# Performance work log

Hardware: AMD Instinct MI355X
Metric: run time of the kernel (lower is better)

Reference implementation:

```python
import jax, jax.numpy as jnp
import numpy as np

D_MODEL, H, DK = 768, 12, 64
RQ, RK, RV = 6, 2, 2
B, S = 8, 4096


def setup_inputs() -> dict:
    key = jax.random.key(0)
    ks = jax.random.split(key, 16)
    def lin(k, din, dout):
        k1, k2 = jax.random.split(k)
        s = 1.0 / np.sqrt(din)
        W = jax.random.uniform(k1, (din, dout), jnp.float32, -s, s)
        b = jax.random.uniform(k2, (dout,), jnp.float32, -s, s)
        return W, b
    W_a_q, b_a_q = lin(ks[0], D_MODEL, H * RQ)
    W_b_q, b_b_q = lin(ks[1], D_MODEL, DK * RQ)
    W_a_k, b_a_k = lin(ks[2], D_MODEL, H * RK)
    W_b_k, b_b_k = lin(ks[3], D_MODEL, DK * RK)
    W_a_v, b_a_v = lin(ks[4], D_MODEL, H * RV)
    W_b_v, b_b_v = lin(ks[5], D_MODEL, DK * RV)
    W_out, b_out = lin(ks[6], H * DK, D_MODEL)
    x = jax.random.normal(ks[7], (B, S, D_MODEL), jnp.float32)
    rope_pos = jax.random.normal(ks[8], (S, DK), jnp.float32)
    return {
        "x": x, "rope_pos": rope_pos,
        "W_a_q": W_a_q, "b_a_q": b_a_q, "W_b_q": W_b_q, "b_b_q": b_b_q,
        "W_a_k": W_a_k, "b_a_k": b_a_k, "W_b_k": W_b_k, "b_b_k": b_b_k,
        "W_a_v": W_a_v, "b_a_v": b_a_v, "W_b_v": W_b_v, "b_b_v": b_b_v,
        "W_out": W_out, "b_out": b_out,
    }


def reference(x, rope_pos, W_a_q, b_a_q, W_b_q, b_b_q, W_a_k, b_a_k,
              W_b_k, b_b_k, W_a_v, b_a_v, W_b_v, b_b_v, W_out, b_out):
    b, s, _ = x.shape
    # factor projections; layout (B, S, rank, feature)
    A_Q = (x @ W_a_q + b_a_q).reshape(b, s, RQ, H)
    B_Q = (x @ W_b_q + b_b_q).reshape(b, s, RQ, DK)
    A_K = (x @ W_a_k + b_a_k).reshape(b, s, RK, H)
    B_K = (x @ W_b_k + b_b_k).reshape(b, s, RK, DK)
    A_V = (x @ W_a_v + b_a_v).reshape(b, s, RV, H)
    B_V = (x @ W_b_v + b_b_v).reshape(b, s, RV, DK)
    rope = rope_pos[None, :, None, :]  # (1,S,1,DK)
    B_Q = B_Q * rope
    B_K = B_K * rope
    # rank-sum outer products -> (B,S,H,DK)
    Q = jnp.einsum('bsrh,bsrd->bshd', A_Q, B_Q)
    K = jnp.einsum('bsrh,bsrd->bshd', A_K, B_K)
    V = jnp.einsum('bsrh,bsrd->bshd', A_V, B_V)
    # faithful to original: scores over head dim, shape (B,S,H,H)
    scores = jnp.einsum('bshd,bsgd->bshg', Q, K) / jnp.sqrt(jnp.float32(DK))
    attn = jax.nn.softmax(scores, axis=-1)
    out = jnp.einsum('bshg,bsgd->bshd', attn, V)  # (B,S,H,DK)
    # faithful reshape: (B,S,H,DK) -> transpose(1,2) -> (B,H,S,DK) -> view (B,S,H*DK)
    out = jnp.transpose(out, (0, 2, 1, 3)).reshape(b, s, H * DK)
    return out @ W_out + b_out
```

## Files before the change

kernel.cpp:

```cpp
#include <hip/hip_runtime.h>
#include <hip/hip_bf16.h>

#define D_MODEL 768
#define NH 12
#define DK 64
#define RQ 6
#define RK 2
#define RV 2
#define BATCH 8
#define SEQ 4096
#define NPOS (BATCH*SEQ)

typedef _Float16 v8h __attribute__((ext_vector_type(8)));
typedef float v4f __attribute__((ext_vector_type(4)));

#define GLDS16(ldst, gsrc)                                                     \
    __builtin_amdgcn_global_load_lds(                                          \
        (const __attribute__((address_space(1))) void*)(unsigned long long)    \
            (const void*)(gsrc),                                               \
        (__attribute__((address_space(3))) void*)(unsigned int)                \
            (unsigned long long)(void*)(ldst),                                 \
        16, 0, 0)

__global__ __launch_bounds__(256) void repack(
    const float* __restrict__ Waq, const float* __restrict__ baq,
    const float* __restrict__ Wbq, const float* __restrict__ bbq,
    const float* __restrict__ Wak, const float* __restrict__ bak,
    const float* __restrict__ Wbk, const float* __restrict__ bbk,
    const float* __restrict__ Wav, const float* __restrict__ bav,
    const float* __restrict__ Wbv, const float* __restrict__ bbv,
    const float* __restrict__ Wo,
    _Float16* __restrict__ WcatT, _Float16* __restrict__ WoT,
    float* __restrict__ bcat)
{
    const int n = blockIdx.x;
    const int t = threadIdx.x;
    const float* W = nullptr; const float* bsrc = nullptr;
    int cols = 0, col = 0;
    if      (n <  72) { W=Waq; bsrc=baq; cols=72;  col=n;     }
    else if (n < 456) { W=Wbq; bsrc=bbq; cols=384; col=n-72;  }
    else if (n < 480) { W=Wak; bsrc=bak; cols=24;  col=n-456; }
    else if (n < 608) { W=Wbk; bsrc=bbk; cols=128; col=n-480; }
    else if (n < 632) { W=Wav; bsrc=bav; cols=24;  col=n-608; }
    else if (n < 760) { W=Wbv; bsrc=bbv; cols=128; col=n-632; }
    for (int k = t; k < 768; k += 256) {
        WcatT[(size_t)n*768 + k] = W ? (_Float16)W[(size_t)k*cols + col] : (_Float16)0.f;
        WoT[(size_t)n*768 + k]   = (_Float16)Wo[(size_t)k*768 + n];
    }
    if (t == 0) bcat[n] = W ? bsrc[col] : 0.f;
}

__global__ __launch_bounds__(256) void convert_x(
    const float4* __restrict__ x, v8h* __restrict__ xh)
{
    const int nth = gridDim.x * 256;
    for (int i = blockIdx.x*256 + threadIdx.x; i < NPOS*96; i += nth) {
        float4 a = x[2*(size_t)i];
        float4 b = x[2*(size_t)i + 1];
        v8h h;
        h[0]=(_Float16)a.x; h[1]=(_Float16)a.y; h[2]=(_Float16)a.z; h[3]=(_Float16)a.w;
        h[4]=(_Float16)b.x; h[5]=(_Float16)b.y; h[6]=(_Float16)b.z; h[7]=(_Float16)b.w;
        xh[i] = h;
    }
}

template<int MODE>
__global__ __launch_bounds__(256) void mfma_gemm(
    const _Float16* __restrict__ A,
    const _Float16* __restrict__ BT,
    const float* __restrict__ bias,
    const float* __restrict__ rope,
    float* __restrict__ C)
{
    const int t = threadIdx.x;
    const int lane = t & 63;
    const int wave = t >> 6;

    const int flat = blockIdx.y * 6 + blockIdx.x;
    const int xcd = flat & 7;
    const int sub = flat >> 3;
    const int ct  = sub % 6;
    const int rt  = xcd * 32 + sub / 6;
    const int row0 = rt * 128;
    const int col0 = ct * 128;

    const int wrow = (wave >> 1) * 64;
    const int wcol = (wave & 1) * 64;

    __shared__ v8h As[512];
    __shared__ v8h Bs[512];

    v4f acc[4][4];
    #pragma unroll
    for (int i = 0; i < 4; ++i)
        #pragma unroll
        for (int j = 0; j < 4; ++j)
            acc[i][j] = (v4f){0.f, 0.f, 0.f, 0.f};

    const v8h* gA = (const v8h*)A;
    const v8h* gB = (const v8h*)BT;

    const int r  = t & 127;
    const int kc = t >> 7;
    const size_t gaBase = (size_t)(row0 + r)*96 + kc;
    const size_t gbBase = (size_t)(col0 + r)*96 + kc;
    char* ldsA = (char*)As + t*16;
    char* ldsB = (char*)Bs + t*16;

    const int q = lane >> 4;
    const int m = lane & 15;

    for (int k0 = 0; k0 < 96; k0 += 4) {
        __syncthreads();
        GLDS16(ldsA,        gA + gaBase + k0);
        GLDS16(ldsA + 4096, gA + gaBase + k0 + 2);
        GLDS16(ldsB,        gB + gbBase + k0);
        GLDS16(ldsB + 4096, gB + gbBase + k0 + 2);
        __syncthreads();

        v8h af[4], bf[4];
        #pragma unroll
        for (int mi = 0; mi < 4; ++mi)
            af[mi] = As[q*128 + wrow + mi*16 + m];
        #pragma unroll
        for (int ni = 0; ni < 4; ++ni)
            bf[ni] = Bs[q*128 + wcol + ni*16 + m];
        #pragma unroll
        for (int mi = 0; mi < 4; ++mi)
            #pragma unroll
            for (int ni = 0; ni < 4; ++ni)
                acc[mi][ni] = __builtin_amdgcn_mfma_f32_16x16x32_f16(
                    af[mi], bf[ni], acc[mi][ni], 0, 0, 0);
    }

    #pragma unroll
    for (int mi = 0; mi < 4; ++mi) {
        #pragma unroll
        for (int i = 0; i < 4; ++i) {
            const int grow = row0 + wrow + mi*16 + q*4 + i;
            #pragma unroll
            for (int ni = 0; ni < 4; ++ni) {
                const int gcol = col0 + wcol + ni*16 + m;
                float v = acc[mi][ni][i] + bias[gcol];
                if (MODE == 0) {
                    const int s = grow & 4095;
                    if (gcol >= 72 && gcol < 456)
                        v *= rope[s*64 + ((gcol - 72) & 63)];
                    else if (gcol >= 480 && gcol < 608)
                        v *= rope[s*64 + ((gcol - 480) & 63)];
                }
                C[(size_t)grow*768 + gcol] = v;
            }
        }
    }
}

__global__ __launch_bounds__(256) void tpa_attn_f(
    const float* __restrict__ P,
    _Float16* __restrict__ O)
{
    const int t = threadIdx.x;
    const int pos0 = blockIdx.x * 8;

    __shared__ float proj[8][772];
    __shared__ float Gs[8][12];
    __shared__ float sc[8][160];
    __shared__ float cs[8][24];

    const float4* gp = (const float4*)P;
    for (int i = t; i < 8*192; i += 256) {
        int p = i / 192, c = i - p*192;
        float4 u = gp[(size_t)(pos0 + p)*192 + c];
        proj[p][c*4+0] = u.x; proj[p][c*4+1] = u.y;
        proj[p][c*4+2] = u.z; proj[p][c*4+3] = u.w;
    }
    __syncthreads();

    if (t < 96) {
        int p = t / 12, u = t - (t/12)*12, r = u >> 1, r2 = u & 1;
        const float* bq = &proj[p][72  + r*64];
        const float* bk = &proj[p][480 + r2*64];
        const int ph = (r*8 + r2*16) & 63;
        float acc = 0.f;
        for (int i = 0; i < 64; ++i) {
            int d = (i + ph) & 63;
            acc = fmaf(bq[d], bk[d], acc);
        }
        Gs[p][u] = acc * 0.125f;
    }
    __syncthreads();

    for (int i = t; i < 8*144; i += 256) {
        int p = i / 144, v = i - p*144, h = v / 12, g = v - (v/12)*12;
        float s = 0.f;
        #pragma unroll
        for (int r = 0; r < RQ; ++r) {
            float mg = fmaf(Gs[p][r*2+1], proj[p][468 + g],
                            Gs[p][r*2+0] * proj[p][456 + g]);
            s = fmaf(proj[p][r*12 + h], mg, s);
        }
        sc[p][h*13 + g] = s;
    }
    __syncthreads();

    if (t < 96) {
        int p = t / 12, h = t - (t/12)*12;
        float* row = &sc[p][h*13];
        float mx = -1e30f;
        #pragma unroll
        for (int g = 0; g < NH; ++g) mx = fmaxf(mx, row[g]);
        float sum = 0.f;
        #pragma unroll
        for (int g = 0; g < NH; ++g) { float e = __expf(row[g]-mx); row[g] = e; sum += e; }
        float inv = 1.0f / sum;
        #pragma unroll
        for (int g = 0; g < NH; ++g) row[g] *= inv;
    }
    __syncthreads();

    if (t < 192) {
        int p = t / 24, u = t - (t/24)*24, h = u >> 1, r2 = u & 1;
        float acc = 0.f;
        #pragma unroll
        for (int g = 0; g < NH; ++g)
            acc = fmaf(sc[p][h*13+g], proj[p][608 + r2*12 + g], acc);
        cs[p][h*2 + r2] = acc;
    }
    __syncthreads();

    for (int i = t; i < 8*768; i += 256) {
        int p = i / 768, j = i - p*768, h = j >> 6, d = j & 63;
        int pos = pos0 + p, b = pos >> 12, s = pos & 4095;
        float val = fmaf(cs[p][h*2+1], proj[p][632 + 64 + d],
                         cs[p][h*2+0] * proj[p][632 + d]);
        O[(((size_t)b*NH + h)*SEQ + s)*DK + d] = (_Float16)val;
    }
}

extern "C" void kernel_launch(void* const* d_in, const int* in_sizes, int n_in,
                              void* d_out, int out_size, void* d_ws, size_t ws_size,
                              hipStream_t stream) {
    const float* x    = (const float*)d_in[0];
    const float* rope = (const float*)d_in[1];
    const float* Waq  = (const float*)d_in[2];
    const float* baq  = (const float*)d_in[3];
    const float* Wbq  = (const float*)d_in[4];
    const float* bbq  = (const float*)d_in[5];
    const float* Wak  = (const float*)d_in[6];
    const float* bak  = (const float*)d_in[7];
    const float* Wbk  = (const float*)d_in[8];
    const float* bbk  = (const float*)d_in[9];
    const float* Wav  = (const float*)d_in[10];
    const float* bav  = (const float*)d_in[11];
    const float* Wbv  = (const float*)d_in[12];
    const float* bbv  = (const float*)d_in[13];
    const float* Wo   = (const float*)d_in[14];
    const float* bo   = (const float*)d_in[15];

    char* ws = (char*)d_ws;
    _Float16* WcatT = (_Float16*)(ws);
    _Float16* WoT   = (_Float16*)(ws + 1179648);
    float*    bcat  = (float*)(ws + 2359296);
    _Float16* O     = (_Float16*)(ws + 2363392);

    float* P = (float*)d_out;

    _Float16* Xh = O;

    repack<<<768, 256, 0, stream>>>(Waq, baq, Wbq, bbq, Wak, bak, Wbk, bbk,
                                    Wav, bav, Wbv, bbv, Wo, WcatT, WoT, bcat);

    convert_x<<<1024, 256, 0, stream>>>((const float4*)x, (v8h*)Xh);

    dim3 gg(6, 256);
    mfma_gemm<0><<<gg, 256, 0, stream>>>(Xh, WcatT, bcat, rope, P);

    tpa_attn_f<<<NPOS/8, 256, 0, stream>>>(P, O);

    mfma_gemm<1><<<gg, 256, 0, stream>>>(O, WoT, bo, nullptr, (float*)d_out);
}
```

Measured before the change: 443.3 us.

## Double-buffer LDS tiles in MFMA GEMM to overlap global loads with compute

The GEMM main loop now uses two LDS buffers per operand and prefetches the next K chunk with global_load_lds while MFMAs run on the current one. Raw s_barrier plus explicit vmcnt waits replace the paired __syncthreads, and s_setprio raises wave priority during the MFMA block. Launch bounds now request 4 blocks per CU. The aim is to hide global memory latency in the K loop, at the cost of doubled LDS use and reliance on hand-managed waitcnt correctness.

```diff
diff --git a/kernel.cpp b/kernel.cpp
--- a/kernel.cpp
+++ b/kernel.cpp
@@ -65,7 +65,7 @@
 }
 
 template<int MODE>
-__global__ __launch_bounds__(256) void mfma_gemm(
+__global__ __launch_bounds__(256, 4) void mfma_gemm(
     const _Float16* __restrict__ A,
     const _Float16* __restrict__ BT,
     const float* __restrict__ bias,
@@ -87,8 +87,8 @@
     const int wrow = (wave >> 1) * 64;
     const int wcol = (wave & 1) * 64;
 
-    __shared__ v8h As[512];
-    __shared__ v8h Bs[512];
+    __shared__ v8h As[2][512];
+    __shared__ v8h Bs[2][512];
 
     v4f acc[4][4];
     #pragma unroll
@@ -104,34 +104,67 @@
     const int kc = t >> 7;
     const size_t gaBase = (size_t)(row0 + r)*96 + kc;
     const size_t gbBase = (size_t)(col0 + r)*96 + kc;
-    char* ldsA = (char*)As + t*16;
-    char* ldsB = (char*)Bs + t*16;
 
     const int q = lane >> 4;
     const int m = lane & 15;
 
-    for (int k0 = 0; k0 < 96; k0 += 4) {
-        __syncthreads();
-        GLDS16(ldsA,        gA + gaBase + k0);
-        GLDS16(ldsA + 4096, gA + gaBase + k0 + 2);
-        GLDS16(ldsB,        gB + gbBase + k0);
-        GLDS16(ldsB + 4096, gB + gbBase + k0 + 2);
-        __syncthreads();
-
-        v8h af[4], bf[4];
-        #pragma unroll
-        for (int mi = 0; mi < 4; ++mi)
-            af[mi] = As[q*128 + wrow + mi*16 + m];
-        #pragma unroll
-        for (int ni = 0; ni < 4; ++ni)
-            bf[ni] = Bs[q*128 + wcol + ni*16 + m];
-        #pragma unroll
-        for (int mi = 0; mi < 4; ++mi)
-            #pragma unroll
-            for (int ni = 0; ni < 4; ++ni)
-                acc[mi][ni] = __builtin_amdgcn_mfma_f32_16x16x32_f16(
-                    af[mi], bf[ni], acc[mi][ni], 0, 0, 0);
-    }
+#define STAGE(buf, kchunk)                                                     \
+    do {                                                                       \
+        char* la_ = (char*)(&As[buf][0]) + t*16;                               \
+        char* lb_ = (char*)(&Bs[buf][0]) + t*16;                               \
+        GLDS16(la_,        gA + gaBase + (kchunk));                            \
+        GLDS16(la_ + 4096, gA + gaBase + (kchunk) + 2);                        \
+        GLDS16(lb_,        gB + gbBase + (kchunk));                            \
+        GLDS16(lb_ + 4096, gB + gbBase + (kchunk) + 2);                        \
+    } while (0)
+
+#define COMPUTE(buf)                                                           \
+    do {                                                                       \
+        v8h af[4], bf[4];                                                      \
+        _Pragma("unroll")                                                      \
+        for (int mi = 0; mi < 4; ++mi)                                         \
+            af[mi] = As[buf][q*128 + wrow + mi*16 + m];                        \
+        _Pragma("unroll")                                                      \
+        for (int ni = 0; ni < 4; ++ni)                                         \
+            bf[ni] = Bs[buf][q*128 + wcol + ni*16 + m];                        \
+        __builtin_amdgcn_s_setprio(1);                                         \
+        _Pragma("unroll")                                                      \
+        for (int mi = 0; mi < 4; ++mi)                                         \
+            _Pragma("unroll")                                                  \
+            for (int ni = 0; ni < 4; ++ni)                                     \
+                acc[mi][ni] = __builtin_amdgcn_mfma_f32_16x16x32_f16(          \
+                    af[mi], bf[ni], acc[mi][ni], 0, 0, 0);                     \
+        __builtin_amdgcn_s_setprio(0);                                         \
+    } while (0)
+
+    STAGE(0, 0);
+
+    for (int t2 = 0; t2 < 12; ++t2) {
+        const int kc0 = t2 * 8;
+
+        STAGE(1, kc0 + 4);
+        asm volatile("s_waitcnt vmcnt(4)" ::: "memory");
+        __builtin_amdgcn_s_barrier();
+        asm volatile("" ::: "memory");
+        COMPUTE(0);
+        asm volatile("" ::: "memory");
+        __builtin_amdgcn_s_barrier();
+
+        if (t2 < 11) {
+            STAGE(0, kc0 + 8);
+            asm volatile("s_waitcnt vmcnt(4)" ::: "memory");
+        } else {
+            asm volatile("s_waitcnt vmcnt(0)" ::: "memory");
+        }
+        __builtin_amdgcn_s_barrier();
+        asm volatile("" ::: "memory");
+        COMPUTE(1);
+        asm volatile("" ::: "memory");
+        __builtin_amdgcn_s_barrier();
+    }
+
+#undef STAGE
+#undef COMPUTE
 
     #pragma unroll
     for (int mi = 0; mi < 4; ++mi) {
```

New measurement: 428.7 us. -3.3%, faster.

## Restructure MFMA GEMM into 256x256 tiles with 4-stage LDS pipeline

Applied to the files above, without the earlier changes.

Replaces the 128x128 tile, 4-wave GEMM with a 256x256 tile, 8-wave kernel that stages K-chunks into a 4-slot LDS ring via direct global-to-LDS loads. Explicit vmcnt waits and barriers interleave LDS reads, async loads and MFMA bursts (with s_setprio raised during the MFMAs), so memory traffic overlaps compute instead of stalling on a double sync each step. This targets global load latency and low data reuse in both projection GEMMs. In exchange it uses 128 KB of LDS, many more accumulator registers and a hand-scheduled wait sequence that is fragile; the grid shrinks to 384 blocks.

```diff
diff --git a/kernel.cpp b/kernel.cpp
--- a/kernel.cpp
+++ b/kernel.cpp
@@ -64,8 +64,13 @@
     }
 }
 
+#define VMCNT(n) asm volatile("s_waitcnt vmcnt(" #n ")" ::: "memory")
+#define BAR() do { asm volatile("" ::: "memory");                              \
+                   __builtin_amdgcn_s_barrier();                               \
+                   asm volatile("" ::: "memory"); } while (0)
+
 template<int MODE>
-__global__ __launch_bounds__(256) void mfma_gemm(
+__global__ __launch_bounds__(512, 2) void mfma_gemm(
     const _Float16* __restrict__ A,
     const _Float16* __restrict__ BT,
     const float* __restrict__ bias,
@@ -75,24 +80,23 @@
     const int t = threadIdx.x;
     const int lane = t & 63;
     const int wave = t >> 6;
-
-    const int flat = blockIdx.y * 6 + blockIdx.x;
+    const int wm = wave >> 2;
+    const int wn = wave & 3;
+
+    const int flat = blockIdx.y * 3 + blockIdx.x;
     const int xcd = flat & 7;
     const int sub = flat >> 3;
-    const int ct  = sub % 6;
-    const int rt  = xcd * 32 + sub / 6;
-    const int row0 = rt * 128;
-    const int col0 = ct * 128;
-
-    const int wrow = (wave >> 1) * 64;
-    const int wcol = (wave & 1) * 64;
-
-    __shared__ v8h As[512];
-    __shared__ v8h Bs[512];
-
-    v4f acc[4][4];
+    const int ct  = sub % 3;
+    const int rt  = xcd * 16 + sub / 3;
+    const int row0 = rt * 256;
+    const int col0 = ct * 256;
+
+    __shared__ v8h As[4][1024];
+    __shared__ v8h Bs[4][1024];
+
+    v4f acc[8][4];
     #pragma unroll
-    for (int i = 0; i < 4; ++i)
+    for (int i = 0; i < 8; ++i)
         #pragma unroll
         for (int j = 0; j < 4; ++j)
             acc[i][j] = (v4f){0.f, 0.f, 0.f, 0.f};
@@ -100,47 +104,82 @@
     const v8h* gA = (const v8h*)A;
     const v8h* gB = (const v8h*)BT;
 
-    const int r  = t & 127;
-    const int kc = t >> 7;
-    const size_t gaBase = (size_t)(row0 + r)*96 + kc;
-    const size_t gbBase = (size_t)(col0 + r)*96 + kc;
-    char* ldsA = (char*)As + t*16;
-    char* ldsB = (char*)Bs + t*16;
+    const size_t gaBase = (size_t)(row0 + (t>>2))*96 + (t&3);
+    const size_t gbBase = (size_t)(col0 + (t>>2))*96 + (t&3);
+    char* ldsA0 = (char*)As + t*16;
+    char* ldsB0 = (char*)Bs + t*16;
 
     const int q = lane >> 4;
     const int m = lane & 15;
-
-    for (int k0 = 0; k0 < 96; k0 += 4) {
-        __syncthreads();
-        GLDS16(ldsA,        gA + gaBase + k0);
-        GLDS16(ldsA + 4096, gA + gaBase + k0 + 2);
-        GLDS16(ldsB,        gB + gbBase + k0);
-        GLDS16(ldsB + 4096, gB + gbBase + k0 + 2);
-        __syncthreads();
-
-        v8h af[4], bf[4];
-        #pragma unroll
-        for (int mi = 0; mi < 4; ++mi)
-            af[mi] = As[q*128 + wrow + mi*16 + m];
-        #pragma unroll
-        for (int ni = 0; ni < 4; ++ni)
-            bf[ni] = Bs[q*128 + wcol + ni*16 + m];
-        #pragma unroll
-        for (int mi = 0; mi < 4; ++mi)
-            #pragma unroll
-            for (int ni = 0; ni < 4; ++ni)
-                acc[mi][ni] = __builtin_amdgcn_mfma_f32_16x16x32_f16(
-                    af[mi], bf[ni], acc[mi][ni], 0, 0, 0);
-    }
+    const int arow4 = (wm*128 + m)*4 + q;
+    const int brow4 = (wn*64  + m)*4 + q;
+
+    v8h af[4], bf[4];
+
+#define STG_A(slot, tile, kc) do {                                             \
+    GLDS16(ldsA0 + (slot)*16384,        gA + gaBase + (tile)*8 + (kc)*4);      \
+    GLDS16(ldsA0 + (slot)*16384 + 8192, gA + gaBase + (tile)*8 + (kc)*4 + 12288); \
+} while (0)
+#define STG_B(slot, tile, kc) do {                                             \
+    GLDS16(ldsB0 + (slot)*16384,        gB + gbBase + (tile)*8 + (kc)*4);      \
+    GLDS16(ldsB0 + (slot)*16384 + 8192, gB + gbBase + (tile)*8 + (kc)*4 + 12288); \
+} while (0)
+#define RD_A_LO(s) { _Pragma("unroll") for (int i_=0;i_<4;++i_) af[i_] = As[s][arow4 + i_*64]; }
+#define RD_A_HI(s) { _Pragma("unroll") for (int i_=0;i_<4;++i_) af[i_] = As[s][arow4 + (i_+4)*64]; }
+#define RD_B(s)    { _Pragma("unroll") for (int i_=0;i_<4;++i_) bf[i_] = Bs[s][brow4 + i_*64]; }
+#define MFMA_Q(mo) do {                                                        \
+    __builtin_amdgcn_s_setprio(1);                                             \
+    _Pragma("unroll")                                                          \
+    for (int mi_=0; mi_<4; ++mi_)                                              \
+        _Pragma("unroll")                                                      \
+        for (int ni_=0; ni_<4; ++ni_)                                          \
+            acc[(mo)+mi_][ni_] = __builtin_amdgcn_mfma_f32_16x16x32_f16(       \
+                af[mi_], bf[ni_], acc[(mo)+mi_][ni_], 0, 0, 0);                \
+    __builtin_amdgcn_s_setprio(0);                                             \
+} while (0)
+
+    STG_A(0, 0, 0); STG_B(0, 0, 0);
+    STG_A(1, 0, 1); STG_B(1, 0, 1);
+    STG_A(2, 1, 0); STG_B(2, 1, 0);
+    VMCNT(6);
+    BAR();
+
+    for (int u = 0; u < 5; ++u) {
+        const int T = 2*u;
+        RD_A_LO(0); RD_B(0); STG_A(3, T+1, 1); BAR(); MFMA_Q(0); BAR();
+        RD_A_HI(0);          STG_B(3, T+1, 1); BAR(); MFMA_Q(4); VMCNT(6); BAR();
+        RD_A_LO(1); RD_B(1); STG_A(0, T+2, 0); BAR(); MFMA_Q(0); BAR();
+        RD_A_HI(1);          STG_B(0, T+2, 0); BAR(); MFMA_Q(4); VMCNT(6); BAR();
+        RD_A_LO(2); RD_B(2); STG_A(1, T+2, 1); BAR(); MFMA_Q(0); BAR();
+        RD_A_HI(2);          STG_B(1, T+2, 1); BAR(); MFMA_Q(4); VMCNT(6); BAR();
+        RD_A_LO(3); RD_B(3); STG_A(2, T+3, 0); BAR(); MFMA_Q(0); BAR();
+        RD_A_HI(3);          STG_B(2, T+3, 0); BAR(); MFMA_Q(4); VMCNT(6); BAR();
+    }
+
+    RD_A_LO(0); RD_B(0); STG_A(3, 11, 1); BAR(); MFMA_Q(0); BAR();
+    RD_A_HI(0);          STG_B(3, 11, 1); BAR(); MFMA_Q(4); VMCNT(6); BAR();
+    RD_A_LO(1); RD_B(1);                  BAR(); MFMA_Q(0); BAR();
+    RD_A_HI(1);                           BAR(); MFMA_Q(4); VMCNT(4); BAR();
+    RD_A_LO(2); RD_B(2);                  BAR(); MFMA_Q(0); BAR();
+    RD_A_HI(2);                           BAR(); MFMA_Q(4); VMCNT(0); BAR();
+    RD_A_LO(3); RD_B(3);                  BAR(); MFMA_Q(0); BAR();
+    RD_A_HI(3);                           BAR(); MFMA_Q(4);
+
+#undef STG_A
+#undef STG_B
+#undef RD_A_LO
+#undef RD_A_HI
+#undef RD_B
+#undef MFMA_Q
 
     #pragma unroll
-    for (int mi = 0; mi < 4; ++mi) {
+    for (int mi = 0; mi < 8; ++mi) {
         #pragma unroll
         for (int i = 0; i < 4; ++i) {
-            const int grow = row0 + wrow + mi*16 + q*4 + i;
+            const int grow = row0 + wm*128 + mi*16 + q*4 + i;
             #pragma unroll
             for (int ni = 0; ni < 4; ++ni) {
-                const int gcol = col0 + wcol + ni*16 + m;
+                const int gcol = col0 + wn*64 + ni*16 + m;
                 float v = acc[mi][ni][i] + bias[gcol];
                 if (MODE == 0) {
                     const int s = grow & 4095;
@@ -272,10 +311,10 @@
 
     convert_x<<<1024, 256, 0, stream>>>((const float4*)x, (v8h*)Xh);
 
-    dim3 gg(6, 256);
-    mfma_gemm<0><<<gg, 256, 0, stream>>>(Xh, WcatT, bcat, rope, P);
+    dim3 gg(3, 128);
+    mfma_gemm<0><<<gg, 512, 0, stream>>>(Xh, WcatT, bcat, rope, P);
 
     tpa_attn_f<<<NPOS/8, 256, 0, stream>>>(P, O);
 
-    mfma_gemm<1><<<gg, 256, 0, stream>>>(O, WoT, bo, nullptr, (float*)d_out);
-}
+    mfma_gemm<1><<<gg, 512, 0, stream>>>(O, WoT, bo, nullptr, (float*)d_out);
+}
```

Result: faster. 419.3 us (-5.4%).

## Replace LDS-staged GEMM tiles with direct register loads and double buffering

Applied to the files above, without the earlier changes.

The GEMM main loop no longer stages A and B tiles through shared memory with global_load_lds and two barriers per k-step. Each wave now loads its MFMA fragments straight from global memory into registers, double-buffered so loads for the next k-step overlap the MFMAs of the current one. MFMA blocks are wrapped in s_setprio, and launch bounds request three blocks per CU. This removes the barriers and LDS traffic, but tiles shared between waves are no longer reused through LDS, so global and L2 load traffic goes up and register pressure rises.

```diff
diff --git a/kernel.cpp b/kernel.cpp
--- a/kernel.cpp
+++ b/kernel.cpp
@@ -13,14 +13,6 @@
 
 typedef _Float16 v8h __attribute__((ext_vector_type(8)));
 typedef float v4f __attribute__((ext_vector_type(4)));
-
-#define GLDS16(ldst, gsrc)                                                     \
-    __builtin_amdgcn_global_load_lds(                                          \
-        (const __attribute__((address_space(1))) void*)(unsigned long long)    \
-            (const void*)(gsrc),                                               \
-        (__attribute__((address_space(3))) void*)(unsigned int)                \
-            (unsigned long long)(void*)(ldst),                                 \
-        16, 0, 0)
 
 __global__ __launch_bounds__(256) void repack(
     const float* __restrict__ Waq, const float* __restrict__ baq,
@@ -65,7 +57,7 @@
 }
 
 template<int MODE>
-__global__ __launch_bounds__(256) void mfma_gemm(
+__global__ __launch_bounds__(256, 3) void mfma_gemm(
     const _Float16* __restrict__ A,
     const _Float16* __restrict__ BT,
     const float* __restrict__ bias,
@@ -87,8 +79,8 @@
     const int wrow = (wave >> 1) * 64;
     const int wcol = (wave & 1) * 64;
 
-    __shared__ v8h As[512];
-    __shared__ v8h Bs[512];
+    const int q = lane >> 4;
+    const int m = lane & 15;
 
     v4f acc[4][4];
     #pragma unroll
@@ -100,38 +92,43 @@
     const v8h* gA = (const v8h*)A;
     const v8h* gB = (const v8h*)BT;
 
-    const int r  = t & 127;
-    const int kc = t >> 7;
-    const size_t gaBase = (size_t)(row0 + r)*96 + kc;
-    const size_t gbBase = (size_t)(col0 + r)*96 + kc;
-    char* ldsA = (char*)As + t*16;
-    char* ldsB = (char*)Bs + t*16;
-
-    const int q = lane >> 4;
-    const int m = lane & 15;
-
-    for (int k0 = 0; k0 < 96; k0 += 4) {
-        __syncthreads();
-        GLDS16(ldsA,        gA + gaBase + k0);
-        GLDS16(ldsA + 4096, gA + gaBase + k0 + 2);
-        GLDS16(ldsB,        gB + gbBase + k0);
-        GLDS16(ldsB + 4096, gB + gbBase + k0 + 2);
-        __syncthreads();
-
-        v8h af[4], bf[4];
-        #pragma unroll
-        for (int mi = 0; mi < 4; ++mi)
-            af[mi] = As[q*128 + wrow + mi*16 + m];
-        #pragma unroll
-        for (int ni = 0; ni < 4; ++ni)
-            bf[ni] = Bs[q*128 + wcol + ni*16 + m];
-        #pragma unroll
-        for (int mi = 0; mi < 4; ++mi)
-            #pragma unroll
-            for (int ni = 0; ni < 4; ++ni)
-                acc[mi][ni] = __builtin_amdgcn_mfma_f32_16x16x32_f16(
-                    af[mi], bf[ni], acc[mi][ni], 0, 0, 0);
-    }
+    const v8h* __restrict__ pA = gA + (size_t)(row0 + wrow + m)*96 + q;
+    const v8h* __restrict__ pB = gB + (size_t)(col0 + wcol + m)*96 + q;
+
+    v8h a0[4], a1[4], b0[4], b1[4];
+
+#define LDF(da, db, ks) do {                                                   \
+    _Pragma("unroll")                                                          \
+    for (int i_ = 0; i_ < 4; ++i_) {                                           \
+        da[i_] = pA[(ks)*4 + i_*1536];                                         \
+        db[i_] = pB[(ks)*4 + i_*1536];                                         \
+    }                                                                          \
+} while (0)
+
+#define MF(a_, b_) do {                                                        \
+    __builtin_amdgcn_s_setprio(1);                                             \
+    _Pragma("unroll")                                                          \
+    for (int mi_ = 0; mi_ < 4; ++mi_)                                          \
+        _Pragma("unroll")                                                      \
+        for (int ni_ = 0; ni_ < 4; ++ni_)                                      \
+            acc[mi_][ni_] = __builtin_amdgcn_mfma_f32_16x16x32_f16(            \
+                a_[mi_], b_[ni_], acc[mi_][ni_], 0, 0, 0);                     \
+    __builtin_amdgcn_s_setprio(0);                                             \
+} while (0)
+
+    LDF(a0, b0, 0);
+    for (int ks = 0; ks < 22; ks += 2) {
+        LDF(a1, b1, ks + 1);
+        MF(a0, b0);
+        LDF(a0, b0, ks + 2);
+        MF(a1, b1);
+    }
+    LDF(a1, b1, 23);
+    MF(a0, b0);
+    MF(a1, b1);
+
+#undef LDF
+#undef MF
 
     #pragma unroll
     for (int mi = 0; mi < 4; ++mi) {
```

New measurement: 545.2 us. +23.0%, slower.
